# Performance work log

Hardware: AMD Instinct MI355X
Metric: run time of the kernel (lower is better)

Reference implementation:

```python
import jax, jax.numpy as jnp
import numpy as np

N, D, H, M = 8192, 64, 4096, 2
EPS = 1e-12  # F.normalize eps


def setup_inputs() -> dict:
    key = jax.random.key(0)
    k0, k1, k2, k3, k4 = jax.random.split(key, 5)
    # spins in {-1, +1}
    x = (2 * jax.random.randint(k0, (N, D), 0, 2) - 1).astype(jnp.float32)
    W1 = jax.random.normal(k1, (D, H), jnp.float32) * 0.05
    b1 = jax.random.normal(k2, (H,), jnp.float32) * 0.05
    W2 = jax.random.normal(k3, (H, M), jnp.float32) * 0.05
    b2 = jax.random.normal(k4, (M,), jnp.float32) * 0.05
    return {"x": x, "W1": W1, "b1": b1, "W2": W2, "b2": b2}


def reference(x, W1, b1, W2, b2):
    # Per step d: mask off sites >= d, run MLP, L2-normalize the 2 amplitudes,
    # select psi_pos/psi_neg by the spin at site d, accumulate product.
    n, d_sites = x.shape
    site_idx = jnp.arange(d_sites)

    def step(wav, d):
        mask = (site_idx < d).astype(x.dtype)          # [D], sites 0..d-1 visible
        h = jnp.tanh((x * mask) @ W1 + b1)             # [N, H]
        out = jnp.tanh(h @ W2 + b2)                    # [N, 2]
        norm = jnp.maximum(
            jnp.sqrt(jnp.sum(out * out, axis=1, keepdims=True)), EPS)
        out = out / norm                               # F.normalize(out, 2)
        sel = jnp.where(x[:, d] > 0, out[:, 0], out[:, 1])
        return wav * sel, None

    wav0 = jnp.ones((n,), x.dtype)
    wav, _ = jax.lax.scan(step, wav0, jnp.arange(d_sites))
    return wav
```

## Files before the change

kernel.cpp:

```cpp
#include <hip/hip_runtime.h>
#include <math.h>

#define NS 8192
#define DS 64
#define HD 4096
#define C2L 2.8853900817779268f
#define CH 8
#define NCH (DS / CH)

typedef float v2f __attribute__((ext_vector_type(2)));

__device__ __forceinline__ v2f pk_add(v2f a, v2f b) {
    v2f d; asm("v_pk_add_f32 %0, %1, %2" : "=v"(d) : "v"(a), "v"(b)); return d;
}
__device__ __forceinline__ v2f pk_mul(v2f a, v2f b) {
    v2f d; asm("v_pk_mul_f32 %0, %1, %2" : "=v"(d) : "v"(a), "v"(b)); return d;
}
__device__ __forceinline__ v2f pk_fma(v2f a, v2f b, v2f c) {
    v2f d; asm("v_pk_fma_f32 %0, %1, %2, %3" : "=v"(d) : "v"(a), "v"(b), "v"(c)); return d;
}

__device__ __forceinline__ float fast_tanh(float x) {
    float t = __builtin_amdgcn_exp2f(x * C2L);
    float r = __builtin_amdgcn_rcpf(t + 1.0f);
    return __builtin_fmaf(-2.0f, r, 1.0f);
}

template <int PATT>
__device__ __forceinline__ v2f swz_xor(v2f v) {
    v2f d;
    d.x = __int_as_float(__builtin_amdgcn_ds_swizzle(__float_as_int(v.x), PATT));
    d.y = __int_as_float(__builtin_amdgcn_ds_swizzle(__float_as_int(v.y), PATT));
    return d;
}

__global__ __launch_bounds__(256) void qnade_prep_E(
    const float* __restrict__ W1, float* __restrict__ Et)
{
    int i = blockIdx.x * 256 + threadIdx.x;
    float w = W1[i] * C2L;
    Et[i]           = __builtin_amdgcn_exp2f(w);
    Et[DS * HD + i] = __builtin_amdgcn_exp2f(-w);
}

__global__ __launch_bounds__(256) void qnade_prep_S(
    const float* __restrict__ W2, const float* __restrict__ b2, float* __restrict__ C01)
{
    __shared__ float p0[4], p1[4];
    int tid = threadIdx.x;
    float s0 = 0.0f, s1 = 0.0f;
    for (int h = tid; h < HD; h += 256) {
        float2 w = ((const float2*)W2)[h];
        s0 += w.x; s1 += w.y;
    }
    #pragma unroll
    for (int m = 1; m < 64; m <<= 1) {
        s0 += __shfl_xor(s0, m, 64);
        s1 += __shfl_xor(s1, m, 64);
    }
    if ((tid & 63) == 0) { p0[tid >> 6] = s0; p1[tid >> 6] = s1; }
    __syncthreads();
    if (tid == 0) {
        C01[0] = p0[0] + p0[1] + p0[2] + p0[3] + b2[0];
        C01[1] = p1[0] + p1[1] + p1[2] + p1[3] + b2[1];
    }
}

__global__ __launch_bounds__(256) void qnade_main(
    const float* __restrict__ x, const float* __restrict__ b1,
    const float* __restrict__ W2, const float* __restrict__ Et,
    const float* __restrict__ C01, float* __restrict__ out)
{
    __shared__ float2 parts[CH][256];
    __shared__ float2 fin[DS];

    const int tid  = threadIdx.x;
    const int lane = tid & 63;
    const int wv   = tid >> 6;
    const int n    = blockIdx.x;
    const int hbase = wv * 1024 + lane * 4;

    v2f w20[8], w21[8];
    #pragma unroll
    for (int q = 0; q < 4; ++q) {
        const float4* p = (const float4*)(W2 + 2 * (hbase + q * 256));
        float4 A = p[0], B = p[1];
        w20[2*q]   = (v2f){A.x, A.z};  w21[2*q]   = (v2f){A.y, A.w};
        w20[2*q+1] = (v2f){B.x, B.z};  w21[2*q+1] = (v2f){B.y, B.w};
    }

    v2f t2[8];
    #pragma unroll
    for (int q = 0; q < 4; ++q) {
        float4 b = *(const float4*)(b1 + hbase + q * 256);
        t2[2*q]   = (v2f){__builtin_amdgcn_exp2f(b.x * C2L), __builtin_amdgcn_exp2f(b.y * C2L)};
        t2[2*q+1] = (v2f){__builtin_amdgcn_exp2f(b.z * C2L), __builtin_amdgcn_exp2f(b.w * C2L)};
    }

    const float xv = x[n * DS + lane];
    const unsigned long long msk = __ballot(xv > 0.0f);

    int d = 0;
    for (int c = 0; c < NCH; ++c) {
        #pragma unroll 2
        for (int s8 = 0; s8 < CH; ++s8, ++d) {
            const unsigned uoff = (((msk >> d) & 1ull) ? 0u : (unsigned)(DS * HD)) + d * HD;
            const float* E = Et + uoff + hbase;
            float4 e0 = *(const float4*)(E);
            float4 e1 = *(const float4*)(E + 256);
            float4 e2 = *(const float4*)(E + 512);
            float4 e3 = *(const float4*)(E + 768);

            v2f p2[8];
            p2[0] = pk_add(t2[0], (v2f){1.0f, 1.0f});
            #pragma unroll
            for (int j = 1; j < 8; ++j) p2[j] = pk_fma(p2[j - 1], t2[j], p2[j - 1]);

            float P = p2[7].x * p2[7].y;
            float R = __builtin_amdgcn_rcpf(P);
            v2f RR = (v2f){R * p2[7].y, R * p2[7].x};

            v2f acc0, acc1;
            {
                v2f r = pk_mul(RR, p2[6]);
                acc0 = pk_mul(r, w20[7]);
                acc1 = pk_mul(r, w21[7]);
                RR = pk_fma(RR, t2[7], RR);
            }
            #pragma unroll
            for (int j = 6; j >= 1; --j) {
                v2f r = pk_mul(RR, p2[j - 1]);
                acc0 = pk_fma(r, w20[j], acc0);
                acc1 = pk_fma(r, w21[j], acc1);
                RR = pk_fma(RR, t2[j], RR);
            }
            acc0 = pk_fma(RR, w20[0], acc0);
            acc1 = pk_fma(RR, w21[0], acc1);

            t2[0] = pk_mul(t2[0], (v2f){e0.x, e0.y});
            t2[1] = pk_mul(t2[1], (v2f){e0.z, e0.w});
            t2[2] = pk_mul(t2[2], (v2f){e1.x, e1.y});
            t2[3] = pk_mul(t2[3], (v2f){e1.z, e1.w});
            t2[4] = pk_mul(t2[4], (v2f){e2.x, e2.y});
            t2[5] = pk_mul(t2[5], (v2f){e2.z, e2.w});
            t2[6] = pk_mul(t2[6], (v2f){e3.x, e3.y});
            t2[7] = pk_mul(t2[7], (v2f){e3.z, e3.w});

            parts[s8][tid] = make_float2(acc0.x + acc0.y, acc1.x + acc1.y);
        }

        __syncthreads();
        {
            const int sr = tid >> 5;
            const int k  = tid & 31;
            v2f s = (v2f){0.0f, 0.0f};
            #pragma unroll
            for (int j = 0; j < 8; ++j) {
                float2 v = parts[sr][k + 32 * j];
                s = pk_add(s, (v2f){v.x, v.y});
            }
            s = pk_add(s, swz_xor<0x041F>(s));
            s = pk_add(s, swz_xor<0x081F>(s));
            s = pk_add(s, swz_xor<0x101F>(s));
            s = pk_add(s, swz_xor<0x201F>(s));
            s = pk_add(s, swz_xor<0x401F>(s));
            if (k == 0) fin[c * CH + sr] = make_float2(s.x, s.y);
        }
        __syncthreads();
    }

    if (tid < DS) {
        const int dd = tid;
        float2 sv = fin[dd];
        float dot0 = __builtin_fmaf(-2.0f, sv.x, C01[0]);
        float dot1 = __builtin_fmaf(-2.0f, sv.y, C01[1]);
        float o0 = fast_tanh(dot0);
        float o1 = fast_tanh(dot1);
        float nrm = sqrtf(__builtin_fmaf(o0, o0, o1 * o1));
        nrm = fmaxf(nrm, 1e-12f);
        float sel = (x[n * DS + dd] > 0.0f) ? o0 : o1;
        float v = sel * __builtin_amdgcn_rcpf(nrm);
        v *= __shfl_xor(v, 1, 64);
        v *= __shfl_xor(v, 2, 64);
        v *= __shfl_xor(v, 4, 64);
        v *= __shfl_xor(v, 8, 64);
        v *= __shfl_xor(v, 16, 64);
        v *= __shfl_xor(v, 32, 64);
        if (tid == 0) out[n] = v;
    }
}

__global__ __launch_bounds__(256) void qnade_fallback(
    const float* __restrict__ x, const float* __restrict__ W1,
    const float* __restrict__ b1, const float* __restrict__ W2,
    const float* __restrict__ b2, float* __restrict__ out)
{
    __shared__ __align__(16) float w20s[HD];
    __shared__ __align__(16) float w21s[HD];
    const int tid = threadIdx.x;
    for (int i = tid; i < HD; i += 256) {
        float2 w = ((const float2*)W2)[i];
        w20s[i] = w.x;
        w21s[i] = w.y;
    }
    const int lane = tid & 63;
    const int wv   = tid >> 6;
    const int n    = (blockIdx.x << 2) + wv;
    const float b20 = b2[0];
    const float b21 = b2[1];
    const float xv = x[n * DS + lane];
    float4 a[16];
    const float4* b1v = (const float4*)b1;
    #pragma unroll
    for (int q = 0; q < 16; ++q) a[q] = b1v[q * 64 + lane];
    __syncthreads();
    const float4* w20v = (const float4*)w20s;
    const float4* w21v = (const float4*)w21s;
    float wav = 1.0f;
    for (int d = 0; d < DS; ++d) {
        const float xd = __shfl(xv, d, 64);
        const float4* w1v = (const float4*)(W1 + d * HD);
        float dot0 = 0.0f, dot1 = 0.0f;
        #pragma unroll
        for (int q = 0; q < 16; ++q) {
            float4 w1 = w1v[q * 64 + lane];
            float4 av = a[q];
            float h0 = fast_tanh(av.x);
            float h1 = fast_tanh(av.y);
            float h2 = fast_tanh(av.z);
            float h3 = fast_tanh(av.w);
            float4 c0 = w20v[q * 64 + lane];
            float4 c1 = w21v[q * 64 + lane];
            dot0 = fmaf(h0, c0.x, dot0); dot0 = fmaf(h1, c0.y, dot0);
            dot0 = fmaf(h2, c0.z, dot0); dot0 = fmaf(h3, c0.w, dot0);
            dot1 = fmaf(h0, c1.x, dot1); dot1 = fmaf(h1, c1.y, dot1);
            dot1 = fmaf(h2, c1.z, dot1); dot1 = fmaf(h3, c1.w, dot1);
            av.x = fmaf(xd, w1.x, av.x); av.y = fmaf(xd, w1.y, av.y);
            av.z = fmaf(xd, w1.z, av.z); av.w = fmaf(xd, w1.w, av.w);
            a[q] = av;
        }
        #pragma unroll
        for (int m = 1; m < 64; m <<= 1) {
            dot0 += __shfl_xor(dot0, m, 64);
            dot1 += __shfl_xor(dot1, m, 64);
        }
        float o0 = fast_tanh(dot0 + b20);
        float o1 = fast_tanh(dot1 + b21);
        float nrm = sqrtf(fmaf(o0, o0, o1 * o1));
        nrm = fmaxf(nrm, 1e-12f);
        float sel = (xd > 0.0f) ? o0 : o1;
        wav *= sel / nrm;
    }
    out[n] = wav;
}

extern "C" void kernel_launch(void* const* d_in, const int* in_sizes, int n_in,
                              void* d_out, int out_size, void* d_ws, size_t ws_size,
                              hipStream_t stream) {
    const float* x  = (const float*)d_in[0];
    const float* W1 = (const float*)d_in[1];
    const float* b1 = (const float*)d_in[2];
    const float* W2 = (const float*)d_in[3];
    const float* b2 = (const float*)d_in[4];
    float* out = (float*)d_out;

    const size_t need = (size_t)(2 * DS * HD + 2) * sizeof(float);
    if (ws_size >= need) {
        float* Et  = (float*)d_ws;
        float* C01 = Et + 2 * DS * HD;
        hipLaunchKernelGGL(qnade_prep_E, dim3(DS * HD / 256), dim3(256), 0, stream, W1, Et);
        hipLaunchKernelGGL(qnade_prep_S, dim3(1), dim3(256), 0, stream, W2, b2, C01);
        hipLaunchKernelGGL(qnade_main, dim3(NS), dim3(256), 0, stream, x, b1, W2, Et, C01, out);
    } else {
        hipLaunchKernelGGL(qnade_fallback, dim3(NS / 4), dim3(256), 0, stream, x, W1, b1, W2, b2, out);
    }
}
```

Before: 423.9 us.

## Process four samples per block to amortize W2 loads and block reductions

Each block now handles four samples and keeps per-sample t2 state in registers, so the W2 and b1 register loads and per-block setup are shared across samples. Partial sums are first reduced within 8-lane groups by swizzles before going to padded shared memory. The chunk grows from 8 to 16 steps to halve the number of barriers. The hidden-unit mapping changes to a contiguous per-thread stride. The cost is much higher register pressure (four copies of t2), with launch bounds requesting two blocks per SM, and a quarter as many blocks.

```diff
diff --git a/kernel.cpp b/kernel.cpp
--- a/kernel.cpp
+++ b/kernel.cpp
@@ -5,8 +5,10 @@
 #define DS 64
 #define HD 4096
 #define C2L 2.8853900817779268f
-#define CH 8
+#define SPB 4
+#define CH 16
 #define NCH (DS / CH)
+#define PPAD 33
 
 typedef float v2f __attribute__((ext_vector_type(2)));
 
@@ -66,119 +68,134 @@
     }
 }
 
-__global__ __launch_bounds__(256) void qnade_main(
+__global__ __launch_bounds__(256, 2) void qnade_main(
     const float* __restrict__ x, const float* __restrict__ b1,
     const float* __restrict__ W2, const float* __restrict__ Et,
     const float* __restrict__ C01, float* __restrict__ out)
 {
-    __shared__ float2 parts[CH][256];
-    __shared__ float2 fin[DS];
+    __shared__ float2 parts[CH][SPB][PPAD];
+    __shared__ float2 fin[SPB][DS];
 
     const int tid  = threadIdx.x;
     const int lane = tid & 63;
     const int wv   = tid >> 6;
-    const int n    = blockIdx.x;
-    const int hbase = wv * 1024 + lane * 4;
+    const int n0   = blockIdx.x * SPB;
+    const int eb   = tid * 4;
 
     v2f w20[8], w21[8];
     #pragma unroll
     for (int q = 0; q < 4; ++q) {
-        const float4* p = (const float4*)(W2 + 2 * (hbase + q * 256));
+        const float4* p = (const float4*)(W2 + 2 * (eb + q * 1024));
         float4 A = p[0], B = p[1];
         w20[2*q]   = (v2f){A.x, A.z};  w21[2*q]   = (v2f){A.y, A.w};
         w20[2*q+1] = (v2f){B.x, B.z};  w21[2*q+1] = (v2f){B.y, B.w};
     }
 
-    v2f t2[8];
+    v2f tinit[8];
     #pragma unroll
     for (int q = 0; q < 4; ++q) {
-        float4 b = *(const float4*)(b1 + hbase + q * 256);
-        t2[2*q]   = (v2f){__builtin_amdgcn_exp2f(b.x * C2L), __builtin_amdgcn_exp2f(b.y * C2L)};
-        t2[2*q+1] = (v2f){__builtin_amdgcn_exp2f(b.z * C2L), __builtin_amdgcn_exp2f(b.w * C2L)};
-    }
-
-    const float xv = x[n * DS + lane];
-    const unsigned long long msk = __ballot(xv > 0.0f);
+        float4 b = *(const float4*)(b1 + eb + q * 1024);
+        tinit[2*q]   = (v2f){__builtin_amdgcn_exp2f(b.x * C2L), __builtin_amdgcn_exp2f(b.y * C2L)};
+        tinit[2*q+1] = (v2f){__builtin_amdgcn_exp2f(b.z * C2L), __builtin_amdgcn_exp2f(b.w * C2L)};
+    }
+    v2f t2[SPB][8];
+    #pragma unroll
+    for (int m = 0; m < SPB; ++m)
+        #pragma unroll
+        for (int j = 0; j < 8; ++j) t2[m][j] = tinit[j];
+
+    unsigned long long msk[SPB];
+    #pragma unroll
+    for (int m = 0; m < SPB; ++m)
+        msk[m] = __ballot(x[(n0 + m) * DS + lane] > 0.0f);
 
     int d = 0;
     for (int c = 0; c < NCH; ++c) {
-        #pragma unroll 2
-        for (int s8 = 0; s8 < CH; ++s8, ++d) {
-            const unsigned uoff = (((msk >> d) & 1ull) ? 0u : (unsigned)(DS * HD)) + d * HD;
-            const float* E = Et + uoff + hbase;
-            float4 e0 = *(const float4*)(E);
-            float4 e1 = *(const float4*)(E + 256);
-            float4 e2 = *(const float4*)(E + 512);
-            float4 e3 = *(const float4*)(E + 768);
-
-            v2f p2[8];
-            p2[0] = pk_add(t2[0], (v2f){1.0f, 1.0f});
+        for (int s16 = 0; s16 < CH; ++s16, ++d) {
             #pragma unroll
-            for (int j = 1; j < 8; ++j) p2[j] = pk_fma(p2[j - 1], t2[j], p2[j - 1]);
-
-            float P = p2[7].x * p2[7].y;
-            float R = __builtin_amdgcn_rcpf(P);
-            v2f RR = (v2f){R * p2[7].y, R * p2[7].x};
-
-            v2f acc0, acc1;
-            {
-                v2f r = pk_mul(RR, p2[6]);
-                acc0 = pk_mul(r, w20[7]);
-                acc1 = pk_mul(r, w21[7]);
-                RR = pk_fma(RR, t2[7], RR);
+            for (int m = 0; m < SPB; ++m) {
+                const unsigned uoff =
+                    (((msk[m] >> d) & 1ull) ? 0u : (unsigned)(DS * HD)) + (unsigned)d * HD;
+                const float* E = Et + uoff + eb;
+                float4 e0 = *(const float4*)(E);
+                float4 e1 = *(const float4*)(E + 1024);
+                float4 e2 = *(const float4*)(E + 2048);
+                float4 e3 = *(const float4*)(E + 3072);
+
+                v2f p2[8];
+                p2[0] = pk_add(t2[m][0], (v2f){1.0f, 1.0f});
+                #pragma unroll
+                for (int j = 1; j < 8; ++j) p2[j] = pk_fma(p2[j - 1], t2[m][j], p2[j - 1]);
+
+                float P = p2[7].x * p2[7].y;
+                float R = __builtin_amdgcn_rcpf(P);
+                v2f RR = (v2f){R * p2[7].y, R * p2[7].x};
+
+                v2f acc0, acc1;
+                {
+                    v2f r = pk_mul(RR, p2[6]);
+                    acc0 = pk_mul(r, w20[7]);
+                    acc1 = pk_mul(r, w21[7]);
+                    RR = pk_fma(RR, t2[m][7], RR);
+                }
+                #pragma unroll
+                for (int j = 6; j >= 1; --j) {
+                    v2f r = pk_mul(RR, p2[j - 1]);
+                    acc0 = pk_fma(r, w20[j], acc0);
+                    acc1 = pk_fma(r, w21[j], acc1);
+                    RR = pk_fma(RR, t2[m][j], RR);
+                }
+                acc0 = pk_fma(RR, w20[0], acc0);
+                acc1 = pk_fma(RR, w21[0], acc1);
+
+                t2[m][0] = pk_mul(t2[m][0], (v2f){e0.x, e0.y});
+                t2[m][1] = pk_mul(t2[m][1], (v2f){e0.z, e0.w});
+                t2[m][2] = pk_mul(t2[m][2], (v2f){e1.x, e1.y});
+                t2[m][3] = pk_mul(t2[m][3], (v2f){e1.z, e1.w});
+                t2[m][4] = pk_mul(t2[m][4], (v2f){e2.x, e2.y});
+                t2[m][5] = pk_mul(t2[m][5], (v2f){e2.z, e2.w});
+                t2[m][6] = pk_mul(t2[m][6], (v2f){e3.x, e3.y});
+                t2[m][7] = pk_mul(t2[m][7], (v2f){e3.z, e3.w});
+
+                v2f s = (v2f){acc0.x + acc0.y, acc1.x + acc1.y};
+                s = pk_add(s, swz_xor<0x041F>(s));
+                s = pk_add(s, swz_xor<0x081F>(s));
+                s = pk_add(s, swz_xor<0x101F>(s));
+                if ((lane & 7) == 0)
+                    parts[s16][m][wv * 8 + (lane >> 3)] = make_float2(s.x, s.y);
             }
-            #pragma unroll
-            for (int j = 6; j >= 1; --j) {
-                v2f r = pk_mul(RR, p2[j - 1]);
-                acc0 = pk_fma(r, w20[j], acc0);
-                acc1 = pk_fma(r, w21[j], acc1);
-                RR = pk_fma(RR, t2[j], RR);
-            }
-            acc0 = pk_fma(RR, w20[0], acc0);
-            acc1 = pk_fma(RR, w21[0], acc1);
-
-            t2[0] = pk_mul(t2[0], (v2f){e0.x, e0.y});
-            t2[1] = pk_mul(t2[1], (v2f){e0.z, e0.w});
-            t2[2] = pk_mul(t2[2], (v2f){e1.x, e1.y});
-            t2[3] = pk_mul(t2[3], (v2f){e1.z, e1.w});
-            t2[4] = pk_mul(t2[4], (v2f){e2.x, e2.y});
-            t2[5] = pk_mul(t2[5], (v2f){e2.z, e2.w});
-            t2[6] = pk_mul(t2[6], (v2f){e3.x, e3.y});
-            t2[7] = pk_mul(t2[7], (v2f){e3.z, e3.w});
-
-            parts[s8][tid] = make_float2(acc0.x + acc0.y, acc1.x + acc1.y);
         }
 
         __syncthreads();
         {
-            const int sr = tid >> 5;
-            const int k  = tid & 31;
+            const int u = tid >> 2;
+            const int j = tid & 3;
+            const int sm = u & (CH - 1);
+            const int m  = u >> 4;
             v2f s = (v2f){0.0f, 0.0f};
             #pragma unroll
-            for (int j = 0; j < 8; ++j) {
-                float2 v = parts[sr][k + 32 * j];
+            for (int i = 0; i < 8; ++i) {
+                float2 v = parts[sm][m][j * 8 + i];
                 s = pk_add(s, (v2f){v.x, v.y});
             }
             s = pk_add(s, swz_xor<0x041F>(s));
             s = pk_add(s, swz_xor<0x081F>(s));
-            s = pk_add(s, swz_xor<0x101F>(s));
-            s = pk_add(s, swz_xor<0x201F>(s));
-            s = pk_add(s, swz_xor<0x401F>(s));
-            if (k == 0) fin[c * CH + sr] = make_float2(s.x, s.y);
+            if (j == 0) fin[m][c * CH + sm] = make_float2(s.x, s.y);
         }
         __syncthreads();
     }
 
-    if (tid < DS) {
-        const int dd = tid;
-        float2 sv = fin[dd];
+    {
+        const int m = wv;
+        float2 sv = fin[m][lane];
         float dot0 = __builtin_fmaf(-2.0f, sv.x, C01[0]);
         float dot1 = __builtin_fmaf(-2.0f, sv.y, C01[1]);
         float o0 = fast_tanh(dot0);
         float o1 = fast_tanh(dot1);
         float nrm = sqrtf(__builtin_fmaf(o0, o0, o1 * o1));
         nrm = fmaxf(nrm, 1e-12f);
-        float sel = (x[n * DS + dd] > 0.0f) ? o0 : o1;
+        bool pos = (msk[m] >> lane) & 1ull;
+        float sel = pos ? o0 : o1;
         float v = sel * __builtin_amdgcn_rcpf(nrm);
         v *= __shfl_xor(v, 1, 64);
         v *= __shfl_xor(v, 2, 64);
@@ -186,7 +203,7 @@
         v *= __shfl_xor(v, 8, 64);
         v *= __shfl_xor(v, 16, 64);
         v *= __shfl_xor(v, 32, 64);
-        if (tid == 0) out[n] = v;
+        if (lane == 0) out[n0 + m] = v;
     }
 }
 
@@ -270,7 +287,7 @@
         float* C01 = Et + 2 * DS * HD;
         hipLaunchKernelGGL(qnade_prep_E, dim3(DS * HD / 256), dim3(256), 0, stream, W1, Et);
         hipLaunchKernelGGL(qnade_prep_S, dim3(1), dim3(256), 0, stream, W2, b2, C01);
-        hipLaunchKernelGGL(qnade_main, dim3(NS), dim3(256), 0, stream, x, b1, W2, Et, C01, out);
+        hipLaunchKernelGGL(qnade_main, dim3(NS / SPB), dim3(256), 0, stream, x, b1, W2, Et, C01, out);
     } else {
         hipLaunchKernelGGL(qnade_fallback, dim3(NS / 4), dim3(256), 0, stream, x, W1, b1, W2, b2, out);
     }
```

Result: slower. 453.1 us (+6.9%).

## Process two samples per block to share W2 registers and amortize syncs

Applied to the files above, without the earlier changes.

Each block now evaluates two spin configurations at once, keeping separate running exp states and sharing the W2 register tile and the per-chunk barriers and reductions between them. The grid is halved and the shared-memory reduction is rearranged to cover both samples. This is meant to amortize per-block setup, barrier, and reduction overhead across two samples and to expose more independent work per thread for latency hiding. In exchange, register pressure roughly doubles for the state arrays, and launch_bounds(256,3) may force spills or lower occupancy.

```diff
diff --git a/kernel.cpp b/kernel.cpp
--- a/kernel.cpp
+++ b/kernel.cpp
@@ -66,18 +66,18 @@
     }
 }
 
-__global__ __launch_bounds__(256) void qnade_main(
+__global__ __launch_bounds__(256, 3) void qnade_main(
     const float* __restrict__ x, const float* __restrict__ b1,
     const float* __restrict__ W2, const float* __restrict__ Et,
     const float* __restrict__ C01, float* __restrict__ out)
 {
-    __shared__ float2 parts[CH][256];
-    __shared__ float2 fin[DS];
+    __shared__ float2 parts[2][CH][256];
+    __shared__ float2 fin[2][DS];
 
     const int tid  = threadIdx.x;
     const int lane = tid & 63;
     const int wv   = tid >> 6;
-    const int n    = blockIdx.x;
+    const int n0   = blockIdx.x * 2;
     const int hbase = wv * 1024 + lane * 4;
 
     v2f w20[8], w21[8];
@@ -89,96 +89,138 @@
         w20[2*q+1] = (v2f){B.x, B.z};  w21[2*q+1] = (v2f){B.y, B.w};
     }
 
-    v2f t2[8];
+    v2f ta[8], tb[8];
     #pragma unroll
     for (int q = 0; q < 4; ++q) {
         float4 b = *(const float4*)(b1 + hbase + q * 256);
-        t2[2*q]   = (v2f){__builtin_amdgcn_exp2f(b.x * C2L), __builtin_amdgcn_exp2f(b.y * C2L)};
-        t2[2*q+1] = (v2f){__builtin_amdgcn_exp2f(b.z * C2L), __builtin_amdgcn_exp2f(b.w * C2L)};
-    }
-
-    const float xv = x[n * DS + lane];
-    const unsigned long long msk = __ballot(xv > 0.0f);
+        v2f v0 = (v2f){__builtin_amdgcn_exp2f(b.x * C2L), __builtin_amdgcn_exp2f(b.y * C2L)};
+        v2f v1 = (v2f){__builtin_amdgcn_exp2f(b.z * C2L), __builtin_amdgcn_exp2f(b.w * C2L)};
+        ta[2*q] = v0; tb[2*q] = v0;
+        ta[2*q+1] = v1; tb[2*q+1] = v1;
+    }
+
+    const unsigned long long mska = __ballot(x[n0 * DS + lane] > 0.0f);
+    const unsigned long long mskb = __ballot(x[(n0 + 1) * DS + lane] > 0.0f);
+    const v2f one = (v2f){1.0f, 1.0f};
 
     int d = 0;
     for (int c = 0; c < NCH; ++c) {
         #pragma unroll 2
         for (int s8 = 0; s8 < CH; ++s8, ++d) {
-            const unsigned uoff = (((msk >> d) & 1ull) ? 0u : (unsigned)(DS * HD)) + d * HD;
-            const float* E = Et + uoff + hbase;
-            float4 e0 = *(const float4*)(E);
-            float4 e1 = *(const float4*)(E + 256);
-            float4 e2 = *(const float4*)(E + 512);
-            float4 e3 = *(const float4*)(E + 768);
-
-            v2f p2[8];
-            p2[0] = pk_add(t2[0], (v2f){1.0f, 1.0f});
-            #pragma unroll
-            for (int j = 1; j < 8; ++j) p2[j] = pk_fma(p2[j - 1], t2[j], p2[j - 1]);
-
-            float P = p2[7].x * p2[7].y;
-            float R = __builtin_amdgcn_rcpf(P);
-            v2f RR = (v2f){R * p2[7].y, R * p2[7].x};
-
-            v2f acc0, acc1;
+            const unsigned rowoff = (unsigned)d * HD;
+            const unsigned ua = (((mska >> d) & 1ull) ? 0u : (unsigned)(DS * HD)) + rowoff;
+            const unsigned ub = (((mskb >> d) & 1ull) ? 0u : (unsigned)(DS * HD)) + rowoff;
+            const float* Ea = Et + ua + hbase;
+            const float* Eb = Et + ub + hbase;
+            float4 ea0 = *(const float4*)(Ea);
+            float4 ea1 = *(const float4*)(Ea + 256);
+            float4 ea2 = *(const float4*)(Ea + 512);
+            float4 ea3 = *(const float4*)(Ea + 768);
+            float4 eb0 = *(const float4*)(Eb);
+            float4 eb1 = *(const float4*)(Eb + 256);
+            float4 eb2 = *(const float4*)(Eb + 512);
+            float4 eb3 = *(const float4*)(Eb + 768);
+
+            v2f pa[8];
+            pa[0] = pk_add(ta[0], one);
+            #pragma unroll
+            for (int j = 1; j < 8; ++j) pa[j] = pk_fma(pa[j - 1], ta[j], pa[j - 1]);
+            float Pa = pa[7].x * pa[7].y;
+            float Ra = __builtin_amdgcn_rcpf(Pa);
+            v2f RA = (v2f){Ra * pa[7].y, Ra * pa[7].x};
+            v2f a0, a1;
             {
-                v2f r = pk_mul(RR, p2[6]);
-                acc0 = pk_mul(r, w20[7]);
-                acc1 = pk_mul(r, w21[7]);
-                RR = pk_fma(RR, t2[7], RR);
+                v2f r = pk_mul(RA, pa[6]);
+                a0 = pk_mul(r, w20[7]);
+                a1 = pk_mul(r, w21[7]);
+                RA = pk_fma(RA, ta[7], RA);
             }
             #pragma unroll
             for (int j = 6; j >= 1; --j) {
-                v2f r = pk_mul(RR, p2[j - 1]);
-                acc0 = pk_fma(r, w20[j], acc0);
-                acc1 = pk_fma(r, w21[j], acc1);
-                RR = pk_fma(RR, t2[j], RR);
-            }
-            acc0 = pk_fma(RR, w20[0], acc0);
-            acc1 = pk_fma(RR, w21[0], acc1);
-
-            t2[0] = pk_mul(t2[0], (v2f){e0.x, e0.y});
-            t2[1] = pk_mul(t2[1], (v2f){e0.z, e0.w});
-            t2[2] = pk_mul(t2[2], (v2f){e1.x, e1.y});
-            t2[3] = pk_mul(t2[3], (v2f){e1.z, e1.w});
-            t2[4] = pk_mul(t2[4], (v2f){e2.x, e2.y});
-            t2[5] = pk_mul(t2[5], (v2f){e2.z, e2.w});
-            t2[6] = pk_mul(t2[6], (v2f){e3.x, e3.y});
-            t2[7] = pk_mul(t2[7], (v2f){e3.z, e3.w});
-
-            parts[s8][tid] = make_float2(acc0.x + acc0.y, acc1.x + acc1.y);
+                v2f r = pk_mul(RA, pa[j - 1]);
+                a0 = pk_fma(r, w20[j], a0);
+                a1 = pk_fma(r, w21[j], a1);
+                RA = pk_fma(RA, ta[j], RA);
+            }
+            a0 = pk_fma(RA, w20[0], a0);
+            a1 = pk_fma(RA, w21[0], a1);
+
+            v2f pb[8];
+            pb[0] = pk_add(tb[0], one);
+            #pragma unroll
+            for (int j = 1; j < 8; ++j) pb[j] = pk_fma(pb[j - 1], tb[j], pb[j - 1]);
+            float Pb = pb[7].x * pb[7].y;
+            float Rb = __builtin_amdgcn_rcpf(Pb);
+            v2f RB = (v2f){Rb * pb[7].y, Rb * pb[7].x};
+            v2f b0, b1a;
+            {
+                v2f r = pk_mul(RB, pb[6]);
+                b0 = pk_mul(r, w20[7]);
+                b1a = pk_mul(r, w21[7]);
+                RB = pk_fma(RB, tb[7], RB);
+            }
+            #pragma unroll
+            for (int j = 6; j >= 1; --j) {
+                v2f r = pk_mul(RB, pb[j - 1]);
+                b0 = pk_fma(r, w20[j], b0);
+                b1a = pk_fma(r, w21[j], b1a);
+                RB = pk_fma(RB, tb[j], RB);
+            }
+            b0 = pk_fma(RB, w20[0], b0);
+            b1a = pk_fma(RB, w21[0], b1a);
+
+            ta[0] = pk_mul(ta[0], (v2f){ea0.x, ea0.y});
+            ta[1] = pk_mul(ta[1], (v2f){ea0.z, ea0.w});
+            ta[2] = pk_mul(ta[2], (v2f){ea1.x, ea1.y});
+            ta[3] = pk_mul(ta[3], (v2f){ea1.z, ea1.w});
+            ta[4] = pk_mul(ta[4], (v2f){ea2.x, ea2.y});
+            ta[5] = pk_mul(ta[5], (v2f){ea2.z, ea2.w});
+            ta[6] = pk_mul(ta[6], (v2f){ea3.x, ea3.y});
+            ta[7] = pk_mul(ta[7], (v2f){ea3.z, ea3.w});
+            tb[0] = pk_mul(tb[0], (v2f){eb0.x, eb0.y});
+            tb[1] = pk_mul(tb[1], (v2f){eb0.z, eb0.w});
+            tb[2] = pk_mul(tb[2], (v2f){eb1.x, eb1.y});
+            tb[3] = pk_mul(tb[3], (v2f){eb1.z, eb1.w});
+            tb[4] = pk_mul(tb[4], (v2f){eb2.x, eb2.y});
+            tb[5] = pk_mul(tb[5], (v2f){eb2.z, eb2.w});
+            tb[6] = pk_mul(tb[6], (v2f){eb3.x, eb3.y});
+            tb[7] = pk_mul(tb[7], (v2f){eb3.z, eb3.w});
+
+            parts[0][s8][tid] = make_float2(a0.x + a0.y, a1.x + a1.y);
+            parts[1][s8][tid] = make_float2(b0.x + b0.y, b1a.x + b1a.y);
         }
 
         __syncthreads();
         {
-            const int sr = tid >> 5;
-            const int k  = tid & 31;
+            const int j  = tid & 15;
+            const int u  = tid >> 4;
+            const int m  = u & 1;
+            const int sr = u >> 1;
             v2f s = (v2f){0.0f, 0.0f};
             #pragma unroll
-            for (int j = 0; j < 8; ++j) {
-                float2 v = parts[sr][k + 32 * j];
+            for (int i = 0; i < 16; ++i) {
+                float2 v = parts[m][sr][j + 16 * i];
                 s = pk_add(s, (v2f){v.x, v.y});
             }
             s = pk_add(s, swz_xor<0x041F>(s));
             s = pk_add(s, swz_xor<0x081F>(s));
             s = pk_add(s, swz_xor<0x101F>(s));
             s = pk_add(s, swz_xor<0x201F>(s));
-            s = pk_add(s, swz_xor<0x401F>(s));
-            if (k == 0) fin[c * CH + sr] = make_float2(s.x, s.y);
+            if (j == 0) fin[m][c * CH + sr] = make_float2(s.x, s.y);
         }
         __syncthreads();
     }
 
-    if (tid < DS) {
-        const int dd = tid;
-        float2 sv = fin[dd];
+    if (wv < 2) {
+        const unsigned long long mm = wv ? mskb : mska;
+        float2 sv = fin[wv][lane];
         float dot0 = __builtin_fmaf(-2.0f, sv.x, C01[0]);
         float dot1 = __builtin_fmaf(-2.0f, sv.y, C01[1]);
         float o0 = fast_tanh(dot0);
         float o1 = fast_tanh(dot1);
         float nrm = sqrtf(__builtin_fmaf(o0, o0, o1 * o1));
         nrm = fmaxf(nrm, 1e-12f);
-        float sel = (x[n * DS + dd] > 0.0f) ? o0 : o1;
+        float sel = ((mm >> lane) & 1ull) ? o0 : o1;
         float v = sel * __builtin_amdgcn_rcpf(nrm);
         v *= __shfl_xor(v, 1, 64);
         v *= __shfl_xor(v, 2, 64);
@@ -186,7 +228,7 @@
         v *= __shfl_xor(v, 8, 64);
         v *= __shfl_xor(v, 16, 64);
         v *= __shfl_xor(v, 32, 64);
-        if (tid == 0) out[n] = v;
+        if (lane == 0) out[n0 + wv] = v;
     }
 }
 
@@ -270,7 +312,7 @@
         float* C01 = Et + 2 * DS * HD;
         hipLaunchKernelGGL(qnade_prep_E, dim3(DS * HD / 256), dim3(256), 0, stream, W1, Et);
         hipLaunchKernelGGL(qnade_prep_S, dim3(1), dim3(256), 0, stream, W2, b2, C01);
-        hipLaunchKernelGGL(qnade_main, dim3(NS), dim3(256), 0, stream, x, b1, W2, Et, C01, out);
+        hipLaunchKernelGGL(qnade_main, dim3(NS / 2), dim3(256), 0, stream, x, b1, W2, Et, C01, out);
     } else {
         hipLaunchKernelGGL(qnade_fallback, dim3(NS / 4), dim3(256), 0, stream, x, W1, b1, W2, b2, out);
     }
```

New measurement: 417.0 us. No clear change (-1.6%).

## Process four samples per block with register-resident weights and prefetched E rows

Applied to the files above, without the earlier changes.

Each block now handles four samples instead of one, so the W2 registers, the b1-derived initial state and the block launch overhead are shared across four independent tanh-product chains. E rows for the next site are loaded one step ahead, hiding global-load latency behind the four chains' arithmetic. The chunk size drops to 4 to fit a 4x-larger partial-sum buffer in LDS, and launch bounds request 2 blocks per CU. The cost is much higher register pressure from 32 live t-vectors plus 16 prefetched float4s, which risks spills or lower occupancy.

```diff
diff --git a/kernel.cpp b/kernel.cpp
--- a/kernel.cpp
+++ b/kernel.cpp
@@ -5,7 +5,7 @@
 #define DS 64
 #define HD 4096
 #define C2L 2.8853900817779268f
-#define CH 8
+#define CH 4
 #define NCH (DS / CH)
 
 typedef float v2f __attribute__((ext_vector_type(2)));
@@ -66,119 +66,152 @@
     }
 }
 
-__global__ __launch_bounds__(256) void qnade_main(
+#define EV(S, N) e##S##N
+#define TV(S, N) t##S##N
+
+#define CHAIN(S, MIDX, SLOT) do {                                             \
+    v2f q1 = pk_add(TV(S,0), one);                                            \
+    v2f q2 = pk_fma(q1, TV(S,1), q1);                                         \
+    v2f q3 = pk_fma(q2, TV(S,2), q2);                                         \
+    v2f q4 = pk_fma(q3, TV(S,3), q3);                                         \
+    v2f q5 = pk_fma(q4, TV(S,4), q4);                                         \
+    v2f q6 = pk_fma(q5, TV(S,5), q5);                                         \
+    v2f q7 = pk_fma(q6, TV(S,6), q6);                                         \
+    v2f q8 = pk_fma(q7, TV(S,7), q7);                                         \
+    float P = q8.x * q8.y;                                                    \
+    float R = __builtin_amdgcn_rcpf(P);                                       \
+    v2f RR = (v2f){R * q8.y, R * q8.x};                                       \
+    v2f r7 = pk_mul(RR, q7);                                                  \
+    v2f A0 = pk_mul(r7, w20[7]);                                              \
+    v2f A1 = pk_mul(r7, w21[7]);                                              \
+    RR = pk_fma(RR, TV(S,7), RR);                                             \
+    v2f r6 = pk_mul(RR, q6); A0 = pk_fma(r6, w20[6], A0); A1 = pk_fma(r6, w21[6], A1); RR = pk_fma(RR, TV(S,6), RR); \
+    v2f r5 = pk_mul(RR, q5); A0 = pk_fma(r5, w20[5], A0); A1 = pk_fma(r5, w21[5], A1); RR = pk_fma(RR, TV(S,5), RR); \
+    v2f r4 = pk_mul(RR, q4); A0 = pk_fma(r4, w20[4], A0); A1 = pk_fma(r4, w21[4], A1); RR = pk_fma(RR, TV(S,4), RR); \
+    v2f r3 = pk_mul(RR, q3); A0 = pk_fma(r3, w20[3], A0); A1 = pk_fma(r3, w21[3], A1); RR = pk_fma(RR, TV(S,3), RR); \
+    v2f r2 = pk_mul(RR, q2); A0 = pk_fma(r2, w20[2], A0); A1 = pk_fma(r2, w21[2], A1); RR = pk_fma(RR, TV(S,2), RR); \
+    v2f r1 = pk_mul(RR, q1); A0 = pk_fma(r1, w20[1], A0); A1 = pk_fma(r1, w21[1], A1); RR = pk_fma(RR, TV(S,1), RR); \
+    A0 = pk_fma(RR, w20[0], A0); A1 = pk_fma(RR, w21[0], A1);                 \
+    parts[SLOT][MIDX][tid] = make_float2(A0.x + A0.y, A1.x + A1.y);           \
+} while (0)
+
+#define TUPD(S) do {                                                          \
+    TV(S,0) = pk_mul(TV(S,0), (v2f){EV(S,0).x, EV(S,0).y});                   \
+    TV(S,1) = pk_mul(TV(S,1), (v2f){EV(S,0).z, EV(S,0).w});                   \
+    TV(S,2) = pk_mul(TV(S,2), (v2f){EV(S,1).x, EV(S,1).y});                   \
+    TV(S,3) = pk_mul(TV(S,3), (v2f){EV(S,1).z, EV(S,1).w});                   \
+    TV(S,4) = pk_mul(TV(S,4), (v2f){EV(S,2).x, EV(S,2).y});                   \
+    TV(S,5) = pk_mul(TV(S,5), (v2f){EV(S,2).z, EV(S,2).w});                   \
+    TV(S,6) = pk_mul(TV(S,6), (v2f){EV(S,3).x, EV(S,3).y});                   \
+    TV(S,7) = pk_mul(TV(S,7), (v2f){EV(S,3).z, EV(S,3).w});                   \
+} while (0)
+
+#define LOADE(S) do {                                                         \
+    unsigned off_ = (((msk##S >> nd) & 1ull) ? 0u : (unsigned)(DS * HD)) + nd * (unsigned)HD; \
+    const float4* ep_ = (const float4*)(Et + off_) + tq;                      \
+    EV(S,0) = ep_[0]; EV(S,1) = ep_[256]; EV(S,2) = ep_[512]; EV(S,3) = ep_[768]; \
+} while (0)
+
+__global__ __launch_bounds__(256, 2) void qnade_main(
     const float* __restrict__ x, const float* __restrict__ b1,
     const float* __restrict__ W2, const float* __restrict__ Et,
     const float* __restrict__ C01, float* __restrict__ out)
 {
-    __shared__ float2 parts[CH][256];
-    __shared__ float2 fin[DS];
+    __shared__ float2 parts[CH][4][256];
+    __shared__ float2 fin[4][DS];
 
     const int tid  = threadIdx.x;
     const int lane = tid & 63;
     const int wv   = tid >> 6;
-    const int n    = blockIdx.x;
-    const int hbase = wv * 1024 + lane * 4;
+    const int n0   = blockIdx.x * 4;
+    const int eb   = tid * 4;
+    const int tq   = tid;
 
     v2f w20[8], w21[8];
     #pragma unroll
     for (int q = 0; q < 4; ++q) {
-        const float4* p = (const float4*)(W2 + 2 * (hbase + q * 256));
+        const float4* p = (const float4*)(W2 + 2 * (eb + q * 1024));
         float4 A = p[0], B = p[1];
         w20[2*q]   = (v2f){A.x, A.z};  w21[2*q]   = (v2f){A.y, A.w};
         w20[2*q+1] = (v2f){B.x, B.z};  w21[2*q+1] = (v2f){B.y, B.w};
     }
 
-    v2f t2[8];
-    #pragma unroll
-    for (int q = 0; q < 4; ++q) {
-        float4 b = *(const float4*)(b1 + hbase + q * 256);
-        t2[2*q]   = (v2f){__builtin_amdgcn_exp2f(b.x * C2L), __builtin_amdgcn_exp2f(b.y * C2L)};
-        t2[2*q+1] = (v2f){__builtin_amdgcn_exp2f(b.z * C2L), __builtin_amdgcn_exp2f(b.w * C2L)};
-    }
-
-    const float xv = x[n * DS + lane];
-    const unsigned long long msk = __ballot(xv > 0.0f);
+    v2f i0, i1, i2, i3, i4, i5, i6, i7;
+    {
+        float4 ba = *(const float4*)(b1 + eb);
+        float4 bb = *(const float4*)(b1 + eb + 1024);
+        float4 bc = *(const float4*)(b1 + eb + 2048);
+        float4 bd = *(const float4*)(b1 + eb + 3072);
+        i0 = (v2f){__builtin_amdgcn_exp2f(ba.x * C2L), __builtin_amdgcn_exp2f(ba.y * C2L)};
+        i1 = (v2f){__builtin_amdgcn_exp2f(ba.z * C2L), __builtin_amdgcn_exp2f(ba.w * C2L)};
+        i2 = (v2f){__builtin_amdgcn_exp2f(bb.x * C2L), __builtin_amdgcn_exp2f(bb.y * C2L)};
+        i3 = (v2f){__builtin_amdgcn_exp2f(bb.z * C2L), __builtin_amdgcn_exp2f(bb.w * C2L)};
+        i4 = (v2f){__builtin_amdgcn_exp2f(bc.x * C2L), __builtin_amdgcn_exp2f(bc.y * C2L)};
+        i5 = (v2f){__builtin_amdgcn_exp2f(bc.z * C2L), __builtin_amdgcn_exp2f(bc.w * C2L)};
+        i6 = (v2f){__builtin_amdgcn_exp2f(bd.x * C2L), __builtin_amdgcn_exp2f(bd.y * C2L)};
+        i7 = (v2f){__builtin_amdgcn_exp2f(bd.z * C2L), __builtin_amdgcn_exp2f(bd.w * C2L)};
+    }
+    v2f tA0=i0,tA1=i1,tA2=i2,tA3=i3,tA4=i4,tA5=i5,tA6=i6,tA7=i7;
+    v2f tB0=i0,tB1=i1,tB2=i2,tB3=i3,tB4=i4,tB5=i5,tB6=i6,tB7=i7;
+    v2f tC0=i0,tC1=i1,tC2=i2,tC3=i3,tC4=i4,tC5=i5,tC6=i6,tC7=i7;
+    v2f tD0=i0,tD1=i1,tD2=i2,tD3=i3,tD4=i4,tD5=i5,tD6=i6,tD7=i7;
+
+    const unsigned long long mskA = __ballot(x[(n0 + 0) * DS + lane] > 0.0f);
+    const unsigned long long mskB = __ballot(x[(n0 + 1) * DS + lane] > 0.0f);
+    const unsigned long long mskC = __ballot(x[(n0 + 2) * DS + lane] > 0.0f);
+    const unsigned long long mskD = __ballot(x[(n0 + 3) * DS + lane] > 0.0f);
+    const v2f one = (v2f){1.0f, 1.0f};
+
+    float4 eA0, eA1, eA2, eA3, eB0, eB1, eB2, eB3;
+    float4 eC0, eC1, eC2, eC3, eD0, eD1, eD2, eD3;
+
+    unsigned nd = 0;
+    LOADE(A); LOADE(B); LOADE(C); LOADE(D);
 
     int d = 0;
-    for (int c = 0; c < NCH; ++c) {
-        #pragma unroll 2
-        for (int s8 = 0; s8 < CH; ++s8, ++d) {
-            const unsigned uoff = (((msk >> d) & 1ull) ? 0u : (unsigned)(DS * HD)) + d * HD;
-            const float* E = Et + uoff + hbase;
-            float4 e0 = *(const float4*)(E);
-            float4 e1 = *(const float4*)(E + 256);
-            float4 e2 = *(const float4*)(E + 512);
-            float4 e3 = *(const float4*)(E + 768);
-
-            v2f p2[8];
-            p2[0] = pk_add(t2[0], (v2f){1.0f, 1.0f});
-            #pragma unroll
-            for (int j = 1; j < 8; ++j) p2[j] = pk_fma(p2[j - 1], t2[j], p2[j - 1]);
-
-            float P = p2[7].x * p2[7].y;
-            float R = __builtin_amdgcn_rcpf(P);
-            v2f RR = (v2f){R * p2[7].y, R * p2[7].x};
-
-            v2f acc0, acc1;
-            {
-                v2f r = pk_mul(RR, p2[6]);
-                acc0 = pk_mul(r, w20[7]);
-                acc1 = pk_mul(r, w21[7]);
-                RR = pk_fma(RR, t2[7], RR);
-            }
-            #pragma unroll
-            for (int j = 6; j >= 1; --j) {
-                v2f r = pk_mul(RR, p2[j - 1]);
-                acc0 = pk_fma(r, w20[j], acc0);
-                acc1 = pk_fma(r, w21[j], acc1);
-                RR = pk_fma(RR, t2[j], RR);
-            }
-            acc0 = pk_fma(RR, w20[0], acc0);
-            acc1 = pk_fma(RR, w21[0], acc1);
-
-            t2[0] = pk_mul(t2[0], (v2f){e0.x, e0.y});
-            t2[1] = pk_mul(t2[1], (v2f){e0.z, e0.w});
-            t2[2] = pk_mul(t2[2], (v2f){e1.x, e1.y});
-            t2[3] = pk_mul(t2[3], (v2f){e1.z, e1.w});
-            t2[4] = pk_mul(t2[4], (v2f){e2.x, e2.y});
-            t2[5] = pk_mul(t2[5], (v2f){e2.z, e2.w});
-            t2[6] = pk_mul(t2[6], (v2f){e3.x, e3.y});
-            t2[7] = pk_mul(t2[7], (v2f){e3.z, e3.w});
-
-            parts[s8][tid] = make_float2(acc0.x + acc0.y, acc1.x + acc1.y);
+    for (int cc = 0; cc < NCH; ++cc) {
+        for (int s4 = 0; s4 < CH; ++s4, ++d) {
+            CHAIN(A, 0, s4);
+            CHAIN(B, 1, s4);
+            CHAIN(C, 2, s4);
+            CHAIN(D, 3, s4);
+            TUPD(A); TUPD(B); TUPD(C); TUPD(D);
+            nd = (unsigned)(d + 1) & (DS - 1);
+            LOADE(A); LOADE(B); LOADE(C); LOADE(D);
         }
 
         __syncthreads();
         {
-            const int sr = tid >> 5;
-            const int k  = tid & 31;
+            const int j  = tid & 15;
+            const int u  = tid >> 4;
+            const int m  = u & 3;
+            const int sr = u >> 2;
             v2f s = (v2f){0.0f, 0.0f};
             #pragma unroll
-            for (int j = 0; j < 8; ++j) {
-                float2 v = parts[sr][k + 32 * j];
+            for (int i = 0; i < 16; ++i) {
+                float2 v = parts[sr][m][j + 16 * i];
                 s = pk_add(s, (v2f){v.x, v.y});
             }
             s = pk_add(s, swz_xor<0x041F>(s));
             s = pk_add(s, swz_xor<0x081F>(s));
             s = pk_add(s, swz_xor<0x101F>(s));
             s = pk_add(s, swz_xor<0x201F>(s));
-            s = pk_add(s, swz_xor<0x401F>(s));
-            if (k == 0) fin[c * CH + sr] = make_float2(s.x, s.y);
+            if (j == 0) fin[m][cc * CH + sr] = make_float2(s.x, s.y);
         }
         __syncthreads();
     }
 
-    if (tid < DS) {
-        const int dd = tid;
-        float2 sv = fin[dd];
+    {
+        const unsigned long long mm = (wv == 0) ? mskA : (wv == 1) ? mskB
+                                    : (wv == 2) ? mskC : mskD;
+        float2 sv = fin[wv][lane];
         float dot0 = __builtin_fmaf(-2.0f, sv.x, C01[0]);
         float dot1 = __builtin_fmaf(-2.0f, sv.y, C01[1]);
         float o0 = fast_tanh(dot0);
         float o1 = fast_tanh(dot1);
         float nrm = sqrtf(__builtin_fmaf(o0, o0, o1 * o1));
         nrm = fmaxf(nrm, 1e-12f);
-        float sel = (x[n * DS + dd] > 0.0f) ? o0 : o1;
+        float sel = ((mm >> lane) & 1ull) ? o0 : o1;
         float v = sel * __builtin_amdgcn_rcpf(nrm);
         v *= __shfl_xor(v, 1, 64);
         v *= __shfl_xor(v, 2, 64);
@@ -186,7 +219,7 @@
         v *= __shfl_xor(v, 8, 64);
         v *= __shfl_xor(v, 16, 64);
         v *= __shfl_xor(v, 32, 64);
-        if (tid == 0) out[n] = v;
+        if (lane == 0) out[n0 + wv] = v;
     }
 }
 
@@ -270,7 +303,7 @@
         float* C01 = Et + 2 * DS * HD;
         hipLaunchKernelGGL(qnade_prep_E, dim3(DS * HD / 256), dim3(256), 0, stream, W1, Et);
         hipLaunchKernelGGL(qnade_prep_S, dim3(1), dim3(256), 0, stream, W2, b2, C01);
-        hipLaunchKernelGGL(qnade_main, dim3(NS), dim3(256), 0, stream, x, b1, W2, Et, C01, out);
+        hipLaunchKernelGGL(qnade_main, dim3(NS / 4), dim3(256), 0, stream, x, b1, W2, Et, C01, out);
     } else {
         hipLaunchKernelGGL(qnade_fallback, dim3(NS / 4), dim3(256), 0, stream, x, W1, b1, W2, b2, out);
     }
```

New measurement: 426.3 us. Within noise of the previous version (+0.6%).
